# Kernel tuning notes

Hardware: AMD Instinct MI355X
Metric: run time of the kernel (lower is better)

## Reference

```python
import jax, jax.numpy as jnp
import numpy as np

HEAD = 8  # number of attention heads (init kwarg)


def setup_inputs() -> dict:
    key = jax.random.key(0)
    k1, k2, k3 = jax.random.split(key, 3)
    b, H, W, c = 8, 32, 32, 512
    dim = 512
    x = jax.random.normal(k1, (b, H, W, c), dtype=jnp.float32)
    # 1x1 Conv == per-pixel matmul over channels
    w_qkv = jax.random.normal(k2, (c, 3 * dim), dtype=jnp.float32) * (c ** -0.5)
    w_out = jax.random.normal(k3, (dim, dim), dtype=jnp.float32) * (dim ** -0.5)
    b_out = jnp.zeros((dim,), dtype=jnp.float32)
    return {"x": x, "w_qkv": w_qkv, "w_out": w_out, "b_out": b_out}


def reference(x, w_qkv, w_out, b_out):
    b, H, W, c = x.shape
    n = H * W
    # QKV 1x1-conv projection (no bias)
    qkv = jnp.einsum('bhwc,cd->bhwd', x, w_qkv)          # (b, H, W, 3*dim)
    qkv = qkv.reshape(b, n, HEAD, -1)                     # (b, n, head, 3*dh)
    q, k, v = jnp.split(qkv, 3, axis=-1)                  # each (b, n, head, dh)
    scale = b ** -0.5  # NOTE: source scales by batch size, reproduced faithfully
    attn = jax.nn.softmax(jnp.einsum('bihd,bjhd->bhij', q, k) * scale, axis=-1)
    out = jnp.einsum('bhij,bjhd->bihd', attn, v)          # (b, n, head, dh)
    out = out.reshape(b, H, W, -1)                        # (b, H, W, dim)
    # output 1x1-conv projection (with bias)
    return jnp.einsum('bhwc,cd->bhwd', out, w_out) + b_out
```

## Files before the change

kernel.cpp:

```cpp
#include <hip/hip_runtime.h>
#include <hip/hip_bf16.h>

typedef __bf16 bf16x8_t __attribute__((ext_vector_type(8)));
typedef float  f32x4_t  __attribute__((ext_vector_type(4)));
typedef short  s16x4_t  __attribute__((ext_vector_type(4)));
typedef short  s16x8_t  __attribute__((ext_vector_type(8)));

#define NTOK   1024
#define CDIM   512
#define QKVDIM 1536
#define NHEAD  8
#define DHEAD  64
#define C1EXP  0.51007088f
#define C2EXP  34.624681f

__device__ __forceinline__ float b2f(short s) {
    unsigned int u = ((unsigned int)(unsigned short)s) << 16;
    float f; __builtin_memcpy(&f, &u, 4); return f;
}
__device__ __forceinline__ short f2b(float f) {
    __bf16 h = (__bf16)f; short s; __builtin_memcpy(&s, &h, 2); return s;
}

__global__ __launch_bounds__(256) void cvt_w(
    const float* __restrict__ wq, const float* __restrict__ wo,
    short* __restrict__ wqbT, short* __restrict__ wobT)
{
    const int b = blockIdx.x;
    const int t = threadIdx.x;
    const int kk = t & 63, grp = t >> 6;
    if (b < 192) {
        const int K0 = (b & 7) * 64, N0 = (b >> 3) * 64;
#pragma unroll
        for (int s = 0; s < 16; ++s) {
            int n = N0 + grp * 16 + s;
            wqbT[(size_t)n * 512 + K0 + kk] = f2b(wq[(size_t)(K0 + kk) * 1536 + n]);
        }
    } else {
        const int b2 = b - 192;
        const int K0 = (b2 & 7) * 64, N0 = (b2 >> 3) * 64;
#pragma unroll
        for (int s = 0; s < 16; ++s) {
            int n = N0 + grp * 16 + s;
            wobT[(size_t)n * 512 + K0 + kk] = f2b(wo[(size_t)(K0 + kk) * 512 + n]);
        }
    }
}

__global__ __launch_bounds__(256) void gemm_qkv(
    const float* __restrict__ X, const short* __restrict__ Bt,
    short* __restrict__ qk, short* __restrict__ vT)
{
    __shared__ __align__(16) short Al[128 * 64];
    __shared__ __align__(16) short Bl[128 * 64];

    const int t = threadIdx.x;
    const int bid = blockIdx.x;
    const int xcd = bid & 7, jpos = bid >> 3;
    const int tm = xcd * 8 + jpos / 12;
    const int tn = jpos % 12;
    const int N0 = tn * 128, M0 = tm * 128;
    const int w = t >> 6, lane = t & 63;
    const int quad = lane >> 4, mr = lane & 15;
    const int wm = (w >> 1) * 64, wn = (w & 1) * 64;

    int srow[4], soff[4];
#pragma unroll
    for (int r = 0; r < 4; ++r) {
        int ci = r * 256 + t;
        srow[r] = ci >> 3;
        soff[r] = (ci & 7) * 8;
    }
    const float* Ag = X  + (size_t)M0 * 512;
    const short* Bg = Bt + (size_t)N0 * 512;

    float4  fa[4][2];
    s16x8_t br[4];
#pragma unroll
    for (int r = 0; r < 4; ++r) {
        const float* pa = Ag + (size_t)srow[r] * 512 + soff[r];
        fa[r][0] = *(const float4*)pa;
        fa[r][1] = *(const float4*)(pa + 4);
        br[r] = *(const s16x8_t*)(Bg + (size_t)srow[r] * 512 + soff[r]);
    }

    f32x4_t acc[4][4];
#pragma unroll
    for (int ms = 0; ms < 4; ++ms)
#pragma unroll
        for (int ns = 0; ns < 4; ++ns) acc[ms][ns] = f32x4_t{0.f,0.f,0.f,0.f};

#pragma unroll 1
    for (int kc = 0; kc < 8; ++kc) {
        __syncthreads();
#pragma unroll
        for (int r = 0; r < 4; ++r) {
            int lds = srow[r] * 64 + (((soff[r] >> 3) ^ (srow[r] & 7)) * 8);
            s16x8_t va;
            va[0] = f2b(fa[r][0].x); va[1] = f2b(fa[r][0].y);
            va[2] = f2b(fa[r][0].z); va[3] = f2b(fa[r][0].w);
            va[4] = f2b(fa[r][1].x); va[5] = f2b(fa[r][1].y);
            va[6] = f2b(fa[r][1].z); va[7] = f2b(fa[r][1].w);
            *(s16x8_t*)(Al + lds) = va;
            *(s16x8_t*)(Bl + lds) = br[r];
        }
        __syncthreads();
        if (kc < 7) {
            int k0 = (kc + 1) * 64;
#pragma unroll
            for (int r = 0; r < 4; ++r) {
                const float* pa = Ag + (size_t)srow[r] * 512 + k0 + soff[r];
                fa[r][0] = *(const float4*)pa;
                fa[r][1] = *(const float4*)(pa + 4);
                br[r] = *(const s16x8_t*)(Bg + (size_t)srow[r] * 512 + k0 + soff[r]);
            }
        }
#pragma unroll
        for (int kh = 0; kh < 2; ++kh) {
            bf16x8_t af[4], bf[4];
#pragma unroll
            for (int ms = 0; ms < 4; ++ms) {
                int rr = wm + ms * 16 + mr;
                af[ms] = *(const bf16x8_t*)(Al + rr * 64 + (((kh * 4 + quad) ^ (rr & 7)) * 8));
            }
#pragma unroll
            for (int ns = 0; ns < 4; ++ns) {
                int rr = wn + ns * 16 + mr;
                bf[ns] = *(const bf16x8_t*)(Bl + rr * 64 + (((kh * 4 + quad) ^ (rr & 7)) * 8));
            }
#pragma unroll
            for (int ms = 0; ms < 4; ++ms)
#pragma unroll
                for (int ns = 0; ns < 4; ++ns)
                    acc[ms][ns] = __builtin_amdgcn_mfma_f32_16x16x32_bf16(
                        af[ms], bf[ns], acc[ms][ns], 0, 0, 0);
        }
    }

#pragma unroll
    for (int ms = 0; ms < 4; ++ms) {
        int row = M0 + wm + ms * 16 + quad * 4;
        int bb = row >> 10, ti = row & 1023;
#pragma unroll
        for (int ns = 0; ns < 4; ++ns) {
            int c0 = N0 + wn + ns * 16;
            int hh = c0 / 192, r0 = c0 % 192;
            if (r0 < 128) {
                size_t base = (size_t)row * 1024 + hh * 128 + r0 + mr;
#pragma unroll
                for (int i = 0; i < 4; ++i)
                    qk[base + (size_t)i * 1024] = f2b(acc[ms][ns][i]);
            } else {
                s16x4_t v4;
#pragma unroll
                for (int i = 0; i < 4; ++i) v4[i] = f2b(acc[ms][ns][i]);
                *(s16x4_t*)(vT + ((size_t)(bb * 8 + hh) * 64 + (r0 - 128) + mr) * 1024 + ti) = v4;
            }
        }
    }
}

template <int N, bool BIAS, bool OUTF32>
__global__ __launch_bounds__(256) void gemm128(
    const short* __restrict__ A, const short* __restrict__ Bt,
    const float* __restrict__ bias, void* __restrict__ C)
{
    __shared__ __align__(16) short Al[128 * 64];
    __shared__ __align__(16) short Bl[128 * 64];

    constexpr int TNT = N / 128;
    const int t = threadIdx.x;
    const int bid = blockIdx.x;
    const int xcd = bid & 7, jpos = bid >> 3;
    const int tm = xcd * 8 + jpos / TNT;
    const int tn = jpos % TNT;
    const int N0 = tn * 128, M0 = tm * 128;
    const int w = t >> 6, lane = t & 63;
    const int quad = lane >> 4, mr = lane & 15;
    const int wm = (w >> 1) * 64, wn = (w & 1) * 64;

    int srow[4], soff[4];
#pragma unroll
    for (int r = 0; r < 4; ++r) {
        int ci = r * 256 + t;
        srow[r] = ci >> 3;
        soff[r] = (ci & 7) * 8;
    }
    const short* Ag = A  + (size_t)M0 * 512;
    const short* Bg = Bt + (size_t)N0 * 512;

    s16x8_t ar[4], br[4];
#pragma unroll
    for (int r = 0; r < 4; ++r) {
        ar[r] = *(const s16x8_t*)(Ag + (size_t)srow[r] * 512 + soff[r]);
        br[r] = *(const s16x8_t*)(Bg + (size_t)srow[r] * 512 + soff[r]);
    }

    f32x4_t acc[4][4];
#pragma unroll
    for (int ms = 0; ms < 4; ++ms)
#pragma unroll
        for (int ns = 0; ns < 4; ++ns) acc[ms][ns] = f32x4_t{0.f,0.f,0.f,0.f};

#pragma unroll 1
    for (int kc = 0; kc < 8; ++kc) {
        __syncthreads();
#pragma unroll
        for (int r = 0; r < 4; ++r) {
            int lds = srow[r] * 64 + (((soff[r] >> 3) ^ (srow[r] & 7)) * 8);
            *(s16x8_t*)(Al + lds) = ar[r];
            *(s16x8_t*)(Bl + lds) = br[r];
        }
        __syncthreads();
        if (kc < 7) {
            int k0 = (kc + 1) * 64;
#pragma unroll
            for (int r = 0; r < 4; ++r) {
                ar[r] = *(const s16x8_t*)(Ag + (size_t)srow[r] * 512 + k0 + soff[r]);
                br[r] = *(const s16x8_t*)(Bg + (size_t)srow[r] * 512 + k0 + soff[r]);
            }
        }
#pragma unroll
        for (int kh = 0; kh < 2; ++kh) {
            bf16x8_t af[4], bf[4];
#pragma unroll
            for (int ms = 0; ms < 4; ++ms) {
                int rr = wm + ms * 16 + mr;
                af[ms] = *(const bf16x8_t*)(Al + rr * 64 + (((kh * 4 + quad) ^ (rr & 7)) * 8));
            }
#pragma unroll
            for (int ns = 0; ns < 4; ++ns) {
                int rr = wn + ns * 16 + mr;
                bf[ns] = *(const bf16x8_t*)(Bl + rr * 64 + (((kh * 4 + quad) ^ (rr & 7)) * 8));
            }
#pragma unroll
            for (int ms = 0; ms < 4; ++ms)
#pragma unroll
                for (int ns = 0; ns < 4; ++ns)
                    acc[ms][ns] = __builtin_amdgcn_mfma_f32_16x16x32_bf16(
                        af[ms], bf[ns], acc[ms][ns], 0, 0, 0);
        }
    }

#pragma unroll
    for (int ms = 0; ms < 4; ++ms) {
        int row = M0 + wm + ms * 16 + quad * 4;
#pragma unroll
        for (int ns = 0; ns < 4; ++ns) {
            int col = N0 + wn + ns * 16 + mr;
            float bz = BIAS ? bias[col] : 0.f;
#pragma unroll
            for (int i = 0; i < 4; ++i) {
                if constexpr (OUTF32)
                    ((float*)C)[(size_t)(row + i) * N + col] = acc[ms][ns][i] + bz;
                else
                    ((short*)C)[(size_t)(row + i) * N + col] = f2b(acc[ms][ns][i]);
            }
        }
    }
}

__global__ __launch_bounds__(512, 4) void attn_st(
    const short* __restrict__ qk, const short* __restrict__ vT,
    short* __restrict__ aout)
{
    __shared__ __align__(16) short Kl[128 * 72];
    __shared__ __align__(16) short Vt[64 * 136];
    __shared__ __align__(16) short Pl[8][16 * 136];

    const int t = threadIdx.x;
    const int g = blockIdx.x;
    const int qt = (g >> 3) & 7;
    const int bh = ((g >> 6) << 3) | (g & 7);
    const int h = bh & 7, b = bh >> 3;
    const int w = t >> 6, lane = t & 63;
    const int quad = lane >> 4, mr = lane & 15;

    const size_t qbase = (size_t)(b * NTOK + qt * 128 + w * 16 + mr) * 1024 + h * 128;
    const bf16x8_t qf0 = *(const bf16x8_t*)(qk + qbase + quad * 8);
    const bf16x8_t qf1 = *(const bf16x8_t*)(qk + qbase + 32 + quad * 8);

    s16x8_t ones_s;
#pragma unroll
    for (int e = 0; e < 8; ++e) ones_s[e] = 0x3F80;
    const bf16x8_t onesv = *(const bf16x8_t*)&ones_s;

    f32x4_t L4 = f32x4_t{0.f, 0.f, 0.f, 0.f};
    f32x4_t O[4];
#pragma unroll
    for (int d = 0; d < 4; ++d) O[d] = f32x4_t{0.f, 0.f, 0.f, 0.f};

    short* Pm = Pl[w];

    const int kr0 = t >> 3, kr1 = kr0 + 64;
    const int kc8 = (t & 7) * 8;
    const int vr0 = t >> 4, vr1 = vr0 + 32;
    const int vc8 = (t & 15) * 8;

    const size_t kg = (size_t)(b * NTOK) * 1024 + h * 128 + 64 + kc8;
    const size_t vg = (size_t)(b * 8 + h) * 64 * 1024 + vc8;

    s16x8_t k0r, k1r, v0r, v1r;
    k0r = *(const s16x8_t*)(qk + kg + (size_t)kr0 * 1024);
    k1r = *(const s16x8_t*)(qk + kg + (size_t)kr1 * 1024);
    v0r = *(const s16x8_t*)(vT + vg + (size_t)vr0 * 1024);
    v1r = *(const s16x8_t*)(vT + vg + (size_t)vr1 * 1024);

#pragma unroll 1
    for (int jt = 0; jt < 8; ++jt) {
        *(s16x8_t*)(Kl + kr0 * 72 + kc8)  = k0r;
        *(s16x8_t*)(Kl + kr1 * 72 + kc8)  = k1r;
        *(s16x8_t*)(Vt + vr0 * 136 + vc8) = v0r;
        *(s16x8_t*)(Vt + vr1 * 136 + vc8) = v1r;
        __syncthreads();

        if (jt < 7) {
            int j0n = (jt + 1) * 128;
            k0r = *(const s16x8_t*)(qk + kg + (size_t)(j0n + kr0) * 1024);
            k1r = *(const s16x8_t*)(qk + kg + (size_t)(j0n + kr1) * 1024);
            v0r = *(const s16x8_t*)(vT + vg + (size_t)vr0 * 1024 + j0n);
            v1r = *(const s16x8_t*)(vT + vg + (size_t)vr1 * 1024 + j0n);
        }

#pragma unroll
        for (int jj = 0; jj < 8; ++jj) {
            const short* kb = Kl + (jj * 16 + mr) * 72 + quad * 8;
            __builtin_amdgcn_s_setprio(1);
            f32x4_t a0 = __builtin_amdgcn_mfma_f32_16x16x32_bf16(
                *(const bf16x8_t*)kb, qf0, f32x4_t{0.f,0.f,0.f,0.f}, 0, 0, 0);
            f32x4_t s = __builtin_amdgcn_mfma_f32_16x16x32_bf16(
                *(const bf16x8_t*)(kb + 32), qf1, a0, 0, 0, 0);
            __builtin_amdgcn_s_setprio(0);
            s16x4_t pv;
#pragma unroll
            for (int r = 0; r < 4; ++r)
                pv[r] = f2b(__builtin_amdgcn_exp2f(s[r] * C1EXP - C2EXP));
            *(s16x4_t*)(Pm + mr * 136 + jj * 16 + quad * 4) = pv;
        }

        bf16x8_t pa[4];
#pragma unroll
        for (int ks = 0; ks < 4; ++ks)
            pa[ks] = *(const bf16x8_t*)(Pm + mr * 136 + ks * 32 + quad * 8);

        __builtin_amdgcn_s_setprio(1);
#pragma unroll
        for (int ks = 0; ks < 4; ++ks)
            L4 = __builtin_amdgcn_mfma_f32_16x16x32_bf16(pa[ks], onesv, L4, 0, 0, 0);
#pragma unroll
        for (int dt = 0; dt < 4; ++dt) {
            const short* vb = Vt + (dt * 16 + mr) * 136 + quad * 8;
#pragma unroll
            for (int ks = 0; ks < 4; ++ks)
                O[dt] = __builtin_amdgcn_mfma_f32_16x16x32_bf16(
                    pa[ks], *(const bf16x8_t*)(vb + ks * 32), O[dt], 0, 0, 0);
        }
        __builtin_amdgcn_s_setprio(0);
        __syncthreads();
    }

#pragma unroll
    for (int dt = 0; dt < 4; ++dt)
#pragma unroll
        for (int i = 0; i < 4; ++i)
            Pm[(quad * 4 + i) * 136 + dt * 16 + mr] = f2b(O[dt][i] * (1.f / L4[i]));
    __syncthreads();

    const int q2 = lane >> 2, h2 = lane & 3;
    const size_t tok = (size_t)(b * NTOK + qt * 128 + w * 16 + q2);
    s16x8_t o0 = *(const s16x8_t*)(Pm + q2 * 136 + h2 * 16);
    s16x8_t o1 = *(const s16x8_t*)(Pm + q2 * 136 + h2 * 16 + 8);
    *(s16x8_t*)(aout + tok * CDIM + h * DHEAD + h2 * 16)     = o0;
    *(s16x8_t*)(aout + tok * CDIM + h * DHEAD + h2 * 16 + 8) = o1;
}

extern "C" void kernel_launch(void* const* d_in, const int* in_sizes, int n_in,
                              void* d_out, int out_size, void* d_ws, size_t ws_size,
                              hipStream_t stream)
{
    const float* x     = (const float*)d_in[0];
    const float* w_qkv = (const float*)d_in[1];
    const float* w_out = (const float*)d_in[2];
    const float* b_out = (const float*)d_in[3];
    for (int i = 0; i < n_in; ++i) {
        if      (in_sizes[i] == 4194304) x     = (const float*)d_in[i];
        else if (in_sizes[i] ==  786432) w_qkv = (const float*)d_in[i];
        else if (in_sizes[i] ==  262144) w_out = (const float*)d_in[i];
        else if (in_sizes[i] ==     512) b_out = (const float*)d_in[i];
    }

    short* qk   = (short*)d_ws;
    short* vT   = (short*)((char*)d_ws + (size_t)8192 * 1024 * 2);
    short* aout = (short*)((char*)d_ws + (size_t)8192 * 1024 * 2 + (size_t)64 * 64 * 1024 * 2);
    short* wobT = (short*)((char*)d_ws + (size_t)33 * 1024 * 1024 + (size_t)1664 * 1024);
    short* wqbT = (short*)d_out + (size_t)8192 * 512;

    cvt_w<<<256, 256, 0, stream>>>(w_qkv, w_out, wqbT, wobT);

    gemm_qkv<<<768, 256, 0, stream>>>(x, wqbT, qk, vT);

    attn_st<<<512, 512, 0, stream>>>(qk, vT, aout);

    gemm128<CDIM, true, true>
        <<<(CDIM / 128) * 64, 256, 0, stream>>>(aout, wobT, b_out, d_out);
}
```

Measured before the change: 135.3 us.

## Process two 16-row query tiles per wave in attention to reuse K/V

```diff
diff --git a/kernel.cpp b/kernel.cpp
--- a/kernel.cpp
+++ b/kernel.cpp
@@ -260,37 +260,43 @@
     }
 }
 
-__global__ __launch_bounds__(512, 4) void attn_st(
+__global__ __launch_bounds__(512, 2) void attn_st(
     const short* __restrict__ qk, const short* __restrict__ vT,
     short* __restrict__ aout)
 {
     __shared__ __align__(16) short Kl[128 * 72];
     __shared__ __align__(16) short Vt[64 * 136];
-    __shared__ __align__(16) short Pl[8][16 * 136];
+    __shared__ __align__(16) short Pl[8][32 * 136];
 
     const int t = threadIdx.x;
     const int g = blockIdx.x;
-    const int qt = (g >> 3) & 7;
-    const int bh = ((g >> 6) << 3) | (g & 7);
-    const int h = bh & 7, b = bh >> 3;
+    const int qt = (g >> 3) & 3;
+    const int h = g & 7, b = g >> 5;
     const int w = t >> 6, lane = t & 63;
     const int quad = lane >> 4, mr = lane & 15;
 
-    const size_t qbase = (size_t)(b * NTOK + qt * 128 + w * 16 + mr) * 1024 + h * 128;
-    const bf16x8_t qf0 = *(const bf16x8_t*)(qk + qbase + quad * 8);
-    const bf16x8_t qf1 = *(const bf16x8_t*)(qk + qbase + 32 + quad * 8);
+    const size_t qra = (size_t)(b * NTOK + qt * 256 + w * 32 + mr) * 1024 + h * 128;
+    const size_t qrb = qra + (size_t)16 * 1024;
+    const bf16x8_t qf0a = *(const bf16x8_t*)(qk + qra + quad * 8);
+    const bf16x8_t qf1a = *(const bf16x8_t*)(qk + qra + 32 + quad * 8);
+    const bf16x8_t qf0b = *(const bf16x8_t*)(qk + qrb + quad * 8);
+    const bf16x8_t qf1b = *(const bf16x8_t*)(qk + qrb + 32 + quad * 8);
 
     s16x8_t ones_s;
 #pragma unroll
     for (int e = 0; e < 8; ++e) ones_s[e] = 0x3F80;
     const bf16x8_t onesv = *(const bf16x8_t*)&ones_s;
 
-    f32x4_t L4 = f32x4_t{0.f, 0.f, 0.f, 0.f};
-    f32x4_t O[4];
-#pragma unroll
-    for (int d = 0; d < 4; ++d) O[d] = f32x4_t{0.f, 0.f, 0.f, 0.f};
-
-    short* Pm = Pl[w];
+    f32x4_t L4a = f32x4_t{0.f,0.f,0.f,0.f}, L4b = f32x4_t{0.f,0.f,0.f,0.f};
+    f32x4_t Oa[4], Ob[4];
+#pragma unroll
+    for (int d = 0; d < 4; ++d) {
+        Oa[d] = f32x4_t{0.f,0.f,0.f,0.f};
+        Ob[d] = f32x4_t{0.f,0.f,0.f,0.f};
+    }
+
+    short* Pma = Pl[w];
+    short* Pmb = Pma + 16 * 136;
 
     const int kr0 = t >> 3, kr1 = kr0 + 64;
     const int kc8 = (t & 7) * 8;
@@ -325,35 +331,50 @@
 #pragma unroll
         for (int jj = 0; jj < 8; ++jj) {
             const short* kb = Kl + (jj * 16 + mr) * 72 + quad * 8;
+            const bf16x8_t kf0 = *(const bf16x8_t*)kb;
+            const bf16x8_t kf1 = *(const bf16x8_t*)(kb + 32);
             __builtin_amdgcn_s_setprio(1);
-            f32x4_t a0 = __builtin_amdgcn_mfma_f32_16x16x32_bf16(
-                *(const bf16x8_t*)kb, qf0, f32x4_t{0.f,0.f,0.f,0.f}, 0, 0, 0);
-            f32x4_t s = __builtin_amdgcn_mfma_f32_16x16x32_bf16(
-                *(const bf16x8_t*)(kb + 32), qf1, a0, 0, 0, 0);
+            f32x4_t a0a = __builtin_amdgcn_mfma_f32_16x16x32_bf16(
+                kf0, qf0a, f32x4_t{0.f,0.f,0.f,0.f}, 0, 0, 0);
+            f32x4_t sa = __builtin_amdgcn_mfma_f32_16x16x32_bf16(
+                kf1, qf1a, a0a, 0, 0, 0);
+            f32x4_t a0b = __builtin_amdgcn_mfma_f32_16x16x32_bf16(
+                kf0, qf0b, f32x4_t{0.f,0.f,0.f,0.f}, 0, 0, 0);
+            f32x4_t sb = __builtin_amdgcn_mfma_f32_16x16x32_bf16(
+                kf1, qf1b, a0b, 0, 0, 0);
             __builtin_amdgcn_s_setprio(0);
-            s16x4_t pv;
-#pragma unroll
-            for (int r = 0; r < 4; ++r)
-                pv[r] = f2b(__builtin_amdgcn_exp2f(s[r] * C1EXP - C2EXP));
-            *(s16x4_t*)(Pm + mr * 136 + jj * 16 + quad * 4) = pv;
-        }
-
-        bf16x8_t pa[4];
-#pragma unroll
-        for (int ks = 0; ks < 4; ++ks)
-            pa[ks] = *(const bf16x8_t*)(Pm + mr * 136 + ks * 32 + quad * 8);
+            s16x4_t pva, pvb;
+#pragma unroll
+            for (int r = 0; r < 4; ++r) {
+                pva[r] = f2b(__builtin_amdgcn_exp2f(sa[r] * C1EXP - C2EXP));
+                pvb[r] = f2b(__builtin_amdgcn_exp2f(sb[r] * C1EXP - C2EXP));
+            }
+            *(s16x4_t*)(Pma + mr * 136 + jj * 16 + quad * 4) = pva;
+            *(s16x4_t*)(Pmb + mr * 136 + jj * 16 + quad * 4) = pvb;
+        }
+
+        bf16x8_t paa[4], pab[4];
+#pragma unroll
+        for (int ks = 0; ks < 4; ++ks) {
+            paa[ks] = *(const bf16x8_t*)(Pma + mr * 136 + ks * 32 + quad * 8);
+            pab[ks] = *(const bf16x8_t*)(Pmb + mr * 136 + ks * 32 + quad * 8);
+        }
 
         __builtin_amdgcn_s_setprio(1);
 #pragma unroll
-        for (int ks = 0; ks < 4; ++ks)
-            L4 = __builtin_amdgcn_mfma_f32_16x16x32_bf16(pa[ks], onesv, L4, 0, 0, 0);
+        for (int ks = 0; ks < 4; ++ks) {
+            L4a = __builtin_amdgcn_mfma_f32_16x16x32_bf16(paa[ks], onesv, L4a, 0, 0, 0);
+            L4b = __builtin_amdgcn_mfma_f32_16x16x32_bf16(pab[ks], onesv, L4b, 0, 0, 0);
+        }
 #pragma unroll
         for (int dt = 0; dt < 4; ++dt) {
             const short* vb = Vt + (dt * 16 + mr) * 136 + quad * 8;
 #pragma unroll
-            for (int ks = 0; ks < 4; ++ks)
-                O[dt] = __builtin_amdgcn_mfma_f32_16x16x32_bf16(
-                    pa[ks], *(const bf16x8_t*)(vb + ks * 32), O[dt], 0, 0, 0);
+            for (int ks = 0; ks < 4; ++ks) {
+                const bf16x8_t vf = *(const bf16x8_t*)(vb + ks * 32);
+                Oa[dt] = __builtin_amdgcn_mfma_f32_16x16x32_bf16(paa[ks], vf, Oa[dt], 0, 0, 0);
+                Ob[dt] = __builtin_amdgcn_mfma_f32_16x16x32_bf16(pab[ks], vf, Ob[dt], 0, 0, 0);
+            }
         }
         __builtin_amdgcn_s_setprio(0);
         __syncthreads();
@@ -362,16 +383,22 @@
 #pragma unroll
     for (int dt = 0; dt < 4; ++dt)
 #pragma unroll
-        for (int i = 0; i < 4; ++i)
-            Pm[(quad * 4 + i) * 136 + dt * 16 + mr] = f2b(O[dt][i] * (1.f / L4[i]));
+        for (int i = 0; i < 4; ++i) {
+            Pma[(quad * 4 + i) * 136 + dt * 16 + mr] = f2b(Oa[dt][i] * (1.f / L4a[i]));
+            Pmb[(quad * 4 + i) * 136 + dt * 16 + mr] = f2b(Ob[dt][i] * (1.f / L4b[i]));
+        }
     __syncthreads();
 
     const int q2 = lane >> 2, h2 = lane & 3;
-    const size_t tok = (size_t)(b * NTOK + qt * 128 + w * 16 + q2);
-    s16x8_t o0 = *(const s16x8_t*)(Pm + q2 * 136 + h2 * 16);
-    s16x8_t o1 = *(const s16x8_t*)(Pm + q2 * 136 + h2 * 16 + 8);
-    *(s16x8_t*)(aout + tok * CDIM + h * DHEAD + h2 * 16)     = o0;
-    *(s16x8_t*)(aout + tok * CDIM + h * DHEAD + h2 * 16 + 8) = o1;
+#pragma unroll
+    for (int it = 0; it < 2; ++it) {
+        const int row = it * 16 + q2;
+        const size_t tok = (size_t)(b * NTOK + qt * 256 + w * 32 + row);
+        s16x8_t o0 = *(const s16x8_t*)(Pma + row * 136 + h2 * 16);
+        s16x8_t o1 = *(const s16x8_t*)(Pma + row * 136 + h2 * 16 + 8);
+        *(s16x8_t*)(aout + tok * CDIM + h * DHEAD + h2 * 16)     = o0;
+        *(s16x8_t*)(aout + tok * CDIM + h * DHEAD + h2 * 16 + 8) = o1;
+    }
 }
 
 extern "C" void kernel_launch(void* const* d_in, const int* in_sizes, int n_in,
@@ -399,7 +426,7 @@
 
     gemm_qkv<<<768, 256, 0, stream>>>(x, wqbT, qk, vT);
 
-    attn_st<<<512, 512, 0, stream>>>(qk, vT, aout);
+    attn_st<<<256, 512, 0, stream>>>(qk, vT, aout);
 
     gemm128<CDIM, true, true>
         <<<(CDIM / 128) * 64, 256, 0, stream>>>(aout, wobT, b_out, d_out);
```

Measured after the change: 131.6 us (median of 2 runs). -2.8%, faster.
